# Performance work log

Hardware: AMD Instinct MI355X
Metric: run time of the kernel (lower is better)

## Reference

```python
import jax, jax.numpy as jnp
import numpy as np

R, C = 30, 56
N = R * C  # 1680
K = 0.005
PRCN = 15
ALPHA = 1.0
BETA = 1.0


def setup_inputs() -> dict:
    key = jax.random.key(0)
    k1, k2 = jax.random.split(key)
    net_in = jax.random.normal(k1, (2 * N,), dtype=jnp.float32)
    # Recurrent connectivity matrix (learned weight in the original, loaded from .mat)
    J = jax.random.normal(k2, (N, N), dtype=jnp.float32) / np.float32(np.sqrt(N))
    return {"net_in": net_in, "J": J}


def reference(net_in, J):
    Iext = net_in[:N].reshape(R, C)
    r0 = net_in[N:2 * N].reshape(R, C)

    def step(r, _):
        # 4-way chunked mm + cat in the original == single matvec J @ r_flat
        temp = (J @ r.reshape(N)).reshape(R, C)
        U = ALPHA * (BETA * temp) + ALPHA * Iext
        sq = jnp.square(0.2 * U)
        recSum = jnp.sum(K * sq)
        # (0.2*U)^2 * (0.04 / recSum) / 0.04  ==  sq / recSum, kept explicit for fidelity
        r_new = sq * (0.04 / recSum) / 0.04
        return r_new, (U, recSum)

    r_last, (Us, sums) = jax.lax.scan(step, r0, None, length=PRCN - 1)
    return Us[-1], sums[-1], r_last
```

## Files before the change

### kernel.cpp

```cpp
#include <hip/hip_runtime.h>


typedef float f32x4 __attribute__((ext_vector_type(4)));

#define N      1680
#define NV4    420
#define NSTEP  14
#define GBLK   105
#define RPB    16
#define RPW    4

__device__ __forceinline__ void jload7(
    const f32x4* p0, const f32x4* p1, const f32x4* p2, const f32x4* p3,
    const f32x4* p4, const f32x4* p5, const f32x4* p6,
    f32x4& v0, f32x4& v1, f32x4& v2, f32x4& v3,
    f32x4& v4, f32x4& v5, f32x4& v6)
{
    asm volatile(
        "global_load_dwordx4 %0, %7, off\n\t"
        "global_load_dwordx4 %1, %8, off\n\t"
        "global_load_dwordx4 %2, %9, off\n\t"
        "global_load_dwordx4 %3, %10, off\n\t"
        "global_load_dwordx4 %4, %11, off\n\t"
        "global_load_dwordx4 %5, %12, off\n\t"
        "global_load_dwordx4 %6, %13, off\n\t"
        "s_waitcnt vmcnt(0)"
        : "=&v"(v0), "=&v"(v1), "=&v"(v2), "=&v"(v3),
          "=&v"(v4), "=&v"(v5), "=&v"(v6)
        : "v"(p0), "v"(p1), "v"(p2), "v"(p3), "v"(p4), "v"(p5), "v"(p6));
}

__device__ __forceinline__ void load7_llc(
    const f32x4* p0, const f32x4* p1, const f32x4* p2, const f32x4* p3,
    const f32x4* p4, const f32x4* p5, const f32x4* p6,
    f32x4& v0, f32x4& v1, f32x4& v2, f32x4& v3,
    f32x4& v4, f32x4& v5, f32x4& v6)
{
    asm volatile(
        "global_load_dwordx4 %0, %7, off sc0 sc1\n\t"
        "global_load_dwordx4 %1, %8, off sc0 sc1\n\t"
        "global_load_dwordx4 %2, %9, off sc0 sc1\n\t"
        "global_load_dwordx4 %3, %10, off sc0 sc1\n\t"
        "global_load_dwordx4 %4, %11, off sc0 sc1\n\t"
        "global_load_dwordx4 %5, %12, off sc0 sc1\n\t"
        "global_load_dwordx4 %6, %13, off sc0 sc1\n\t"
        "s_waitcnt vmcnt(0)"
        : "=&v"(v0), "=&v"(v1), "=&v"(v2), "=&v"(v3),
          "=&v"(v4), "=&v"(v5), "=&v"(v6)
        : "v"(p0), "v"(p1), "v"(p2), "v"(p3), "v"(p4), "v"(p5), "v"(p6)
        : "memory");
}

__device__ __forceinline__ void llc_store4(f32x4* p, f32x4 v) {
    asm volatile("global_store_dwordx4 %0, %1, off sc0 sc1"
                 :: "v"(p), "v"(v) : "memory");
}

__global__ __launch_bounds__(256, 1) void fused_recur(
    const float* __restrict__ J,
    const float* __restrict__ net_in,
    float* __restrict__ out,
    float* __restrict__ ws)
{
    f32x4* bufs = (f32x4*)ws;

    const int tid  = threadIdx.x;
    const int lane = tid & 63;
    const int wave = tid >> 6;
    const int row0 = (int)blockIdx.x * RPB + wave * RPW;

    const unsigned pend0 = (lane < 36) ? 0x7Fu : 0x3Fu;

    f32x4 Jr[RPW][7];
    #pragma unroll
    for (int m = 0; m < RPW; ++m) {
        const f32x4* jb = (const f32x4*)(J + (size_t)(row0 + m) * N);
        jload7(jb + lane,       jb + lane + 64,  jb + lane + 128,
               jb + lane + 192, jb + lane + 256, jb + lane + 320,
               (lane < 36) ? (jb + lane + 384) : jb,
               Jr[m][0], Jr[m][1], Jr[m][2], Jr[m][3],
               Jr[m][4], Jr[m][5], Jr[m][6]);
    }

    float iext[RPW];
    #pragma unroll
    for (int m = 0; m < RPW; ++m) iext[m] = net_in[row0 + m];

    float Uv[RPW], Qv[RPW];

    #pragma unroll 1
    for (int t = 0; t < NSTEP; ++t) {
        f32x4 acc[RPW];
        #pragma unroll
        for (int m = 0; m < RPW; ++m) acc[m] = (f32x4)0.f;
        float psum = 0.0f;

        if (t == 0) {
            const f32x4* r0 = (const f32x4*)(net_in + N);
            #pragma unroll
            for (int k = 0; k < 7; ++k) {
                const int idx = lane + 64 * k;
                const f32x4 q = (idx < NV4) ? r0[idx] : (f32x4)0.f;
                #pragma unroll
                for (int m = 0; m < RPW; ++m) {
                    acc[m][0] += Jr[m][k][0] * q[0];
                    acc[m][1] += Jr[m][k][1] * q[1];
                    acc[m][2] += Jr[m][k][2] * q[2];
                    acc[m][3] += Jr[m][k][3] * q[3];
                }
            }
        } else {
            const f32x4* base = bufs + (size_t)(t - 1) * NV4;
            const f32x4* q0 = base + lane;
            const f32x4* q1 = base + lane + 64;
            const f32x4* q2 = base + lane + 128;
            const f32x4* q3 = base + lane + 192;
            const f32x4* q4 = base + lane + 256;
            const f32x4* q5 = base + lane + 320;
            const f32x4* q6 = (lane < 36) ? (base + lane + 384) : base;

            unsigned pend = pend0;
            for (;;) {
                f32x4 rv[7];
                load7_llc(q0, q1, q2, q3, q4, q5, q6,
                          rv[0], rv[1], rv[2], rv[3], rv[4], rv[5], rv[6]);
                #pragma unroll
                for (int k = 0; k < 7; ++k) {
                    if ((pend >> k) & 1u) {
                        const f32x4 q = rv[k];
                        const float mn = fminf(fminf(q[0], q[1]),
                                               fminf(q[2], q[3]));
                        if (mn >= 0.0f) {
                            #pragma unroll
                            for (int m = 0; m < RPW; ++m) {
                                acc[m][0] += Jr[m][k][0] * q[0];
                                acc[m][1] += Jr[m][k][1] * q[1];
                                acc[m][2] += Jr[m][k][2] * q[2];
                                acc[m][3] += Jr[m][k][3] * q[3];
                            }
                            psum += (q[0] + q[1]) + (q[2] + q[3]);
                            pend &= ~(1u << k);
                        }
                    }
                }
                if (!__any((int)pend)) break;
                __builtin_amdgcn_s_sleep(1);
            }
        }

        float red[5];
        #pragma unroll
        for (int m = 0; m < RPW; ++m)
            red[m] = (acc[m][0] + acc[m][1]) + (acc[m][2] + acc[m][3]);
        red[4] = psum;
        #pragma unroll
        for (int off = 32; off; off >>= 1) {
            #pragma unroll
            for (int i = 0; i < 5; ++i) red[i] += __shfl_xor(red[i], off, 64);
        }
        const float inv = (t == 0) ? 1.0f : 1.0f / (0.005f * red[4]);

        #pragma unroll
        for (int m = 0; m < RPW; ++m) {
            const float U  = red[m] * inv + iext[m];
            const float u2 = 0.2f * U;
            Uv[m] = U;
            Qv[m] = u2 * u2;
        }

        if (lane == 0) {
            f32x4 pub = { Qv[0], Qv[1], Qv[2], Qv[3] };
            llc_store4(bufs + (size_t)t * NV4 + (row0 >> 2), pub);
        }
    }

    float s13;
    {
        const f32x4* base = bufs + (size_t)(NSTEP - 1) * NV4;
        const f32x4* q0 = base + lane;
        const f32x4* q1 = base + lane + 64;
        const f32x4* q2 = base + lane + 128;
        const f32x4* q3 = base + lane + 192;
        const f32x4* q4 = base + lane + 256;
        const f32x4* q5 = base + lane + 320;
        const f32x4* q6 = (lane < 36) ? (base + lane + 384) : base;

        unsigned pend = pend0;
        float psum = 0.0f;
        for (;;) {
            f32x4 rv[7];
            load7_llc(q0, q1, q2, q3, q4, q5, q6,
                      rv[0], rv[1], rv[2], rv[3], rv[4], rv[5], rv[6]);
            #pragma unroll
            for (int k = 0; k < 7; ++k) {
                if ((pend >> k) & 1u) {
                    const f32x4 q = rv[k];
                    const float mn = fminf(fminf(q[0], q[1]),
                                           fminf(q[2], q[3]));
                    if (mn >= 0.0f) {
                        psum += (q[0] + q[1]) + (q[2] + q[3]);
                        pend &= ~(1u << k);
                    }
                }
            }
            if (!__any((int)pend)) break;
            __builtin_amdgcn_s_sleep(1);
        }
        #pragma unroll
        for (int off = 32; off; off >>= 1) psum += __shfl_xor(psum, off, 64);
        s13 = 0.005f * psum;
    }

    if (lane == 0) {
        f32x4 u4 = { Uv[0], Uv[1], Uv[2], Uv[3] };
        *(f32x4*)(out + row0) = u4;
    }
    if (lane < RPW) {
        const float q = (lane == 0) ? Qv[0] : (lane == 1) ? Qv[1]
                       : (lane == 2) ? Qv[2] : Qv[3];
        out[N + 1 + row0 + lane] = q / s13;
    }
    if (blockIdx.x == 0 && tid == 0) out[N] = s13;
}

extern "C" void kernel_launch(void* const* d_in, const int* in_sizes, int n_in,
                              void* d_out, int out_size, void* d_ws, size_t ws_size,
                              hipStream_t stream) {
    const float* net_in = (const float*)d_in[0];
    const float* J      = (const float*)d_in[1];
    hipMemsetAsync(d_ws, 0xBF, (size_t)NSTEP * NV4 * sizeof(f32x4), stream);
    fused_recur<<<GBLK, 256, 0, stream>>>(J, net_in, (float*)d_out, (float*)d_ws);
}
```

Measured before the change: 122.4 us.

## Stream J rows each step and relay polled vector through LDS from one wave

Rather than keeping the J rows resident in registers, each step re-issues the J loads without waiting, so their latency overlaps the cross-block poll. Only wave 0 polls the global LLC buffer for the previous step's vector. It copies the vector into double-buffered LDS and raises a workgroup-scope flag that the other waves spin on. The poll loop also loses its s_sleep. The aim is less polling traffic to the LLC and lower register pressure, at the cost of reloading J from cache every step and adding an intra-block spin dependency on wave 0.

```diff
diff --git a/kernel.cpp b/kernel.cpp
--- a/kernel.cpp
+++ b/kernel.cpp
@@ -10,7 +10,7 @@
 #define RPB    16
 #define RPW    4
 
-__device__ __forceinline__ void jload7(
+__device__ __forceinline__ void jload7_issue(
     const f32x4* p0, const f32x4* p1, const f32x4* p2, const f32x4* p3,
     const f32x4* p4, const f32x4* p5, const f32x4* p6,
     f32x4& v0, f32x4& v1, f32x4& v2, f32x4& v3,
@@ -23,11 +23,15 @@
         "global_load_dwordx4 %3, %10, off\n\t"
         "global_load_dwordx4 %4, %11, off\n\t"
         "global_load_dwordx4 %5, %12, off\n\t"
-        "global_load_dwordx4 %6, %13, off\n\t"
-        "s_waitcnt vmcnt(0)"
+        "global_load_dwordx4 %6, %13, off"
         : "=&v"(v0), "=&v"(v1), "=&v"(v2), "=&v"(v3),
           "=&v"(v4), "=&v"(v5), "=&v"(v6)
         : "v"(p0), "v"(p1), "v"(p2), "v"(p3), "v"(p4), "v"(p5), "v"(p6));
+}
+
+__device__ __forceinline__ void vm_wait0() {
+    asm volatile("s_waitcnt vmcnt(0)" ::: "memory");
+    __builtin_amdgcn_sched_barrier(0);
 }
 
 __device__ __forceinline__ void load7_llc(
@@ -62,6 +66,9 @@
     float* __restrict__ out,
     float* __restrict__ ws)
 {
+    __shared__ f32x4 lds_r[2][NV4];
+    __shared__ float lds_flag[16];
+
     f32x4* bufs = (f32x4*)ws;
 
     const int tid  = threadIdx.x;
@@ -71,45 +78,45 @@
 
     const unsigned pend0 = (lane < 36) ? 0x7Fu : 0x3Fu;
 
-    f32x4 Jr[RPW][7];
-    #pragma unroll
-    for (int m = 0; m < RPW; ++m) {
-        const f32x4* jb = (const f32x4*)(J + (size_t)(row0 + m) * N);
-        jload7(jb + lane,       jb + lane + 64,  jb + lane + 128,
-               jb + lane + 192, jb + lane + 256, jb + lane + 320,
-               (lane < 36) ? (jb + lane + 384) : jb,
-               Jr[m][0], Jr[m][1], Jr[m][2], Jr[m][3],
-               Jr[m][4], Jr[m][5], Jr[m][6]);
-    }
+    if (tid < 16) lds_flag[tid] = 0.0f;
+    __syncthreads();
 
     float iext[RPW];
     #pragma unroll
     for (int m = 0; m < RPW; ++m) iext[m] = net_in[row0 + m];
 
+    const f32x4* jb[RPW];
+    #pragma unroll
+    for (int m = 0; m < RPW; ++m)
+        jb[m] = (const f32x4*)(J + (size_t)(row0 + m) * N);
+
     float Uv[RPW], Qv[RPW];
 
     #pragma unroll 1
     for (int t = 0; t < NSTEP; ++t) {
-        f32x4 acc[RPW];
-        #pragma unroll
-        for (int m = 0; m < RPW; ++m) acc[m] = (f32x4)0.f;
+        f32x4 Jr[RPW][7];
+        #pragma unroll
+        for (int m = 0; m < RPW; ++m)
+            jload7_issue(jb[m] + lane,       jb[m] + lane + 64,
+                         jb[m] + lane + 128, jb[m] + lane + 192,
+                         jb[m] + lane + 256, jb[m] + lane + 320,
+                         (lane < 36) ? (jb[m] + lane + 384) : jb[m],
+                         Jr[m][0], Jr[m][1], Jr[m][2], Jr[m][3],
+                         Jr[m][4], Jr[m][5], Jr[m][6]);
+
+        f32x4 rv[7];
         float psum = 0.0f;
+        const int par = (t - 1) & 1;
 
         if (t == 0) {
+            vm_wait0();
             const f32x4* r0 = (const f32x4*)(net_in + N);
             #pragma unroll
             for (int k = 0; k < 7; ++k) {
                 const int idx = lane + 64 * k;
-                const f32x4 q = (idx < NV4) ? r0[idx] : (f32x4)0.f;
-                #pragma unroll
-                for (int m = 0; m < RPW; ++m) {
-                    acc[m][0] += Jr[m][k][0] * q[0];
-                    acc[m][1] += Jr[m][k][1] * q[1];
-                    acc[m][2] += Jr[m][k][2] * q[2];
-                    acc[m][3] += Jr[m][k][3] * q[3];
-                }
-            }
-        } else {
+                rv[k] = (idx < NV4) ? r0[idx] : (f32x4)0.f;
+            }
+        } else if (wave == 0) {
             const f32x4* base = bufs + (size_t)(t - 1) * NV4;
             const f32x4* q0 = base + lane;
             const f32x4* q1 = base + lane + 64;
@@ -120,8 +127,8 @@
             const f32x4* q6 = (lane < 36) ? (base + lane + 384) : base;
 
             unsigned pend = pend0;
+            #pragma unroll 1
             for (;;) {
-                f32x4 rv[7];
                 load7_llc(q0, q1, q2, q3, q4, q5, q6,
                           rv[0], rv[1], rv[2], rv[3], rv[4], rv[5], rv[6]);
                 #pragma unroll
@@ -131,23 +138,47 @@
                         const float mn = fminf(fminf(q[0], q[1]),
                                                fminf(q[2], q[3]));
                         if (mn >= 0.0f) {
-                            #pragma unroll
-                            for (int m = 0; m < RPW; ++m) {
-                                acc[m][0] += Jr[m][k][0] * q[0];
-                                acc[m][1] += Jr[m][k][1] * q[1];
-                                acc[m][2] += Jr[m][k][2] * q[2];
-                                acc[m][3] += Jr[m][k][3] * q[3];
-                            }
-                            psum += (q[0] + q[1]) + (q[2] + q[3]);
+                            lds_r[par][lane + 64 * k] = q;
                             pend &= ~(1u << k);
                         }
                     }
                 }
-                if (!__any((int)pend)) break;
-                __builtin_amdgcn_s_sleep(1);
-            }
-        }
-
+                if (!__any(pend != 0u)) break;
+            }
+            if (lane == 0)
+                __hip_atomic_store(&lds_flag[t - 1], 1.0f, __ATOMIC_RELEASE,
+                                   __HIP_MEMORY_SCOPE_WORKGROUP);
+            if (lane >= 36) rv[6] = (f32x4)0.f;
+            #pragma unroll
+            for (int k = 0; k < 7; ++k)
+                psum += (rv[k][0] + rv[k][1]) + (rv[k][2] + rv[k][3]);
+        } else {
+            while (__hip_atomic_load(&lds_flag[t - 1], __ATOMIC_ACQUIRE,
+                                     __HIP_MEMORY_SCOPE_WORKGROUP) == 0.0f) {}
+            vm_wait0();
+            #pragma unroll
+            for (int k = 0; k < 7; ++k) {
+                const int idx = lane + 64 * k;
+                rv[k] = (idx < NV4) ? lds_r[par][idx] : (f32x4)0.f;
+            }
+            #pragma unroll
+            for (int k = 0; k < 7; ++k)
+                psum += (rv[k][0] + rv[k][1]) + (rv[k][2] + rv[k][3]);
+        }
+
+        f32x4 acc[RPW];
+        #pragma unroll
+        for (int m = 0; m < RPW; ++m) acc[m] = (f32x4)0.f;
+        #pragma unroll
+        for (int k = 0; k < 7; ++k) {
+            #pragma unroll
+            for (int m = 0; m < RPW; ++m) {
+                acc[m][0] += Jr[m][k][0] * rv[k][0];
+                acc[m][1] += Jr[m][k][1] * rv[k][1];
+                acc[m][2] += Jr[m][k][2] * rv[k][2];
+                acc[m][3] += Jr[m][k][3] * rv[k][3];
+            }
+        }
         float red[5];
         #pragma unroll
         for (int m = 0; m < RPW; ++m)
@@ -175,7 +206,7 @@
     }
 
     float s13;
-    {
+    if (wave == 0) {
         const f32x4* base = bufs + (size_t)(NSTEP - 1) * NV4;
         const f32x4* q0 = base + lane;
         const f32x4* q1 = base + lane + 64;
@@ -184,31 +215,37 @@
         const f32x4* q4 = base + lane + 256;
         const f32x4* q5 = base + lane + 320;
         const f32x4* q6 = (lane < 36) ? (base + lane + 384) : base;
-
+        f32x4 rv[7];
         unsigned pend = pend0;
         float psum = 0.0f;
+        #pragma unroll 1
         for (;;) {
-            f32x4 rv[7];
             load7_llc(q0, q1, q2, q3, q4, q5, q6,
                       rv[0], rv[1], rv[2], rv[3], rv[4], rv[5], rv[6]);
             #pragma unroll
             for (int k = 0; k < 7; ++k) {
                 if ((pend >> k) & 1u) {
                     const f32x4 q = rv[k];
-                    const float mn = fminf(fminf(q[0], q[1]),
-                                           fminf(q[2], q[3]));
+                    const float mn = fminf(fminf(q[0], q[1]), fminf(q[2], q[3]));
                     if (mn >= 0.0f) {
                         psum += (q[0] + q[1]) + (q[2] + q[3]);
                         pend &= ~(1u << k);
                     }
                 }
             }
-            if (!__any((int)pend)) break;
-            __builtin_amdgcn_s_sleep(1);
+            if (!__any(pend != 0u)) break;
         }
         #pragma unroll
         for (int off = 32; off; off >>= 1) psum += __shfl_xor(psum, off, 64);
         s13 = 0.005f * psum;
+        if (lane == 0)
+            __hip_atomic_store(&lds_flag[15], s13, __ATOMIC_RELEASE,
+                               __HIP_MEMORY_SCOPE_WORKGROUP);
+    } else {
+        float f;
+        while ((f = __hip_atomic_load(&lds_flag[15], __ATOMIC_ACQUIRE,
+                                      __HIP_MEMORY_SCOPE_WORKGROUP)) == 0.0f) {}
+        s13 = f;
     }
 
     if (lane == 0) {
```

Result: faster. 111.3 us (-9.1%).
